# Performance work log

Hardware: AMD Instinct MI355X
Metric: run time of the kernel (lower is better)

Reference implementation:

```python
import jax, jax.numpy as jnp
import numpy as np


def _add_self_loops(src, dst, n):
    loop = jnp.arange(n, dtype=src.dtype)
    return jnp.concatenate([src, loop]), jnp.concatenate([dst, loop])


def _graph_conv(x, src, dst, n, W, b):
    # DGL GraphConv with norm='both':
    #   h = D_in^{-1/2} * A^T * (D_out^{-1/2} * x) @ W + b
    ones = jnp.ones(src.shape, dtype=x.dtype)
    deg_out = jax.ops.segment_sum(ones, src, num_segments=n)
    deg_in = jax.ops.segment_sum(ones, dst, num_segments=n)
    norm_s = jax.lax.rsqrt(jnp.maximum(deg_out, 1.0))
    norm_d = jax.lax.rsqrt(jnp.maximum(deg_in, 1.0))
    msg = (x * norm_s[:, None])[src]                      # [E, d] gather
    agg = jax.ops.segment_sum(msg, dst, num_segments=n)   # [N, d] scatter-add
    return (agg * norm_d[:, None]) @ W + b


def _ntype_forward(x, src, dst, W0, b0, W1, b1):
    n = x.shape[0]
    src, dst = _add_self_loops(src, dst, n)  # dgl.add_self_loop each layer; graph is static
    h = _graph_conv(x, src, dst, n, W0, b0)
    h = jax.nn.relu(h)  # dropout skipped: eval mode (training=False)
    h = _graph_conv(h, src, dst, n, W1, b1)
    return h


def setup_inputs() -> dict:
    key = jax.random.key(0)
    ks = jax.random.split(key, 16)
    NA, NB, EA, EB = 50000, 30000, 600000, 300000
    DA, DB, H = 256, 128, 128
    s = 0.05
    return {
        "feat_a": jax.random.normal(ks[0], (NA, DA), jnp.float32),
        "feat_b": jax.random.normal(ks[1], (NB, DB), jnp.float32),
        "src_a": jax.random.randint(ks[2], (EA,), 0, NA),
        "dst_a": jax.random.randint(ks[3], (EA,), 0, NA),
        "src_b": jax.random.randint(ks[4], (EB,), 0, NB),
        "dst_b": jax.random.randint(ks[5], (EB,), 0, NB),
        "Wa0": jax.random.normal(ks[6], (DA, H), jnp.float32) * s,
        "ba0": jnp.zeros((H,), jnp.float32),
        "Wa1": jax.random.normal(ks[7], (H, H), jnp.float32) * s,
        "ba1": jnp.zeros((H,), jnp.float32),
        "Wb0": jax.random.normal(ks[8], (DB, H), jnp.float32) * s,
        "bb0": jnp.zeros((H,), jnp.float32),
        "Wb1": jax.random.normal(ks[9], (H, H), jnp.float32) * s,
        "bb1": jnp.zeros((H,), jnp.float32),
    }


def reference(feat_a, feat_b, src_a, dst_a, src_b, dst_b,
              Wa0, ba0, Wa1, ba1, Wb0, bb0, Wb1, bb1):
    h_a = _ntype_forward(feat_a, src_a, dst_a, Wa0, ba0, Wa1, ba1)
    h_b = _ntype_forward(feat_b, src_b, dst_b, Wb0, bb0, Wb1, bb1)
    return h_a, h_b
```

## Files before the change

### kernel.cpp

```cpp
#include <hip/hip_runtime.h>
#include <hip/hip_bf16.h>

#define H 128
#define BK 64
#define LDSTR 72

#define EPB 2048
#define BUCK_BITS 8
#define BUCK 256

typedef _Float16 f16;
typedef unsigned int u32;
typedef __attribute__((ext_vector_type(8))) _Float16 f16x8;
typedef __attribute__((ext_vector_type(4))) _Float16 f16x4;
typedef __attribute__((ext_vector_type(4))) float floatx4;

static inline __host__ int ceil_div(int a, int b) { return (a + b - 1) / b; }

__global__ __launch_bounds__(256) void p1K(
    const int* __restrict__ sA, const int* __restrict__ dA, int EA, int nblkA, int nbinsA,
    const int* __restrict__ sB, const int* __restrict__ dB, int EB, int nblkB, int nbinsB,
    int* __restrict__ ch, int offAd, int offBd, int offAs, int offBs, int Lall,
    const float* __restrict__ Wa0, f16* ta0, const float* __restrict__ Wa1, f16* ta1,
    const float* __restrict__ Wb0, f16* tb0, const float* __restrict__ Wb1, f16* tb1, int DA) {
    __shared__ int bd[BUCK], bs[BUCK];
    int bid = blockIdx.x, t = threadIdx.x;
    int p1n = nblkA + nblkB;
    if (bid < p1n) {
        const int *src, *dst; int E, nblk, nbins, blk, od, os;
        if (bid < nblkA) { src = sA; dst = dA; E = EA; nblk = nblkA; nbins = nbinsA; blk = bid; od = offAd; os = offAs; }
        else { src = sB; dst = dB; E = EB; nblk = nblkB; nbins = nbinsB; blk = bid - nblkA; od = offBd; os = offBs; }
        bd[t] = 0; bs[t] = 0;
        __syncthreads();
        int e0 = blk * EPB, e1 = min(E, e0 + EPB);
        for (int e = e0 + t; e < e1; e += 256) {
            atomicAdd(&bd[dst[e] >> BUCK_BITS], 1);
            atomicAdd(&bs[src[e] >> BUCK_BITS], 1);
        }
        __syncthreads();
        for (int b = t; b < nbins; b += 256) {
            ch[od + b * nblk + blk] = bd[b];
            ch[os + b * nblk + blk] = bs[b];
        }
        if (bid == 0 && t == 0) ch[Lall] = 0;
    } else {
        int b2 = bid - p1n;
        int k2 = b2 * 2 + (t >> 7);
        const float* W; f16* T; int D, k;
        if (k2 < DA) { W = Wa0; T = ta0; D = DA; k = k2; }
        else if (k2 < DA + H) { W = Wa1; T = ta1; D = H; k = k2 - DA; }
        else if (k2 < DA + 2 * H) { W = Wb0; T = tb0; D = H; k = k2 - DA - H; }
        else { W = Wb1; T = tb1; D = H; k = k2 - DA - 2 * H; }
        int c = t & 127;
        T[(size_t)c * D + k] = (f16)W[(size_t)k * H + c];
    }
}

__global__ __launch_bounds__(256) void scan1K(int* __restrict__ ch, int n, int* __restrict__ bsum) {
    __shared__ int sh[256];
    int t = threadIdx.x;
    int base = blockIdx.x * 1024 + t * 4;
    int v[4];
#pragma unroll
    for (int i = 0; i < 4; i++) v[i] = (base + i < n) ? ch[base + i] : 0;
    int s = v[0] + v[1] + v[2] + v[3];
    sh[t] = s;
    __syncthreads();
    for (int off = 1; off < 256; off <<= 1) {
        int x = (t >= off) ? sh[t - off] : 0;
        __syncthreads();
        sh[t] += x;
        __syncthreads();
    }
    int run = sh[t] - s;
#pragma unroll
    for (int i = 0; i < 4; i++) {
        if (base + i < n) ch[base + i] = run;
        run += v[i];
    }
    if (t == 255) bsum[blockIdx.x] = sh[255];
}

__global__ __launch_bounds__(256) void scan23K(int* __restrict__ ch, const int* __restrict__ bsum,
                                               int nb, int n) {
    __shared__ int sh[256];
    int t = threadIdx.x;
    int v = (t < nb) ? bsum[t] : 0;
    sh[t] = v;
    __syncthreads();
    for (int off = 1; off < 256; off <<= 1) {
        int x = (t >= off) ? sh[t - off] : 0;
        __syncthreads();
        sh[t] += x;
        __syncthreads();
    }
    int k = blockIdx.x >> 2;
    int add = (k == 0) ? 0 : sh[k - 1];
    int i = blockIdx.x * 256 + t;
    if (i < n) ch[i] += add;
}

__global__ __launch_bounds__(256) void p3K(
    const int* __restrict__ sA, const int* __restrict__ dA, int EA, int nblkA, int nbinsA,
    const int* __restrict__ sB, const int* __restrict__ dB, int EB, int nblkB, int nbinsB,
    const int* __restrict__ ch, int offAd, int offBd, int offAs, int offBs,
    u32* __restrict__ binned) {
    __shared__ int cd[BUCK], cs[BUCK], ofd[BUCK], ofs[BUCK];
    const int *src, *dst; int E, nblk, nbins, blk, od, os;
    if ((int)blockIdx.x < nblkA) {
        src = sA; dst = dA; E = EA; nblk = nblkA; nbins = nbinsA; blk = blockIdx.x; od = offAd; os = offAs;
    } else {
        src = sB; dst = dB; E = EB; nblk = nblkB; nbins = nbinsB; blk = blockIdx.x - nblkA; od = offBd; os = offBs;
    }
    int t = threadIdx.x;
    cd[t] = 0; cs[t] = 0;
    if (t < nbins) {
        ofd[t] = ch[od + t * nblk + blk];
        ofs[t] = ch[os + t * nblk + blk];
    }
    __syncthreads();
    int e0 = blk * EPB, e1 = min(E, e0 + EPB);
    for (int e = e0 + t; e < e1; e += 256) {
        int d = dst[e], s = src[e];
        int b = d >> BUCK_BITS;
        int r = atomicAdd(&cd[b], 1);
        binned[ofd[b] + r] = (u32)s | ((u32)(d & (BUCK - 1)) << 16);
        int b2 = s >> BUCK_BITS;
        int r2 = atomicAdd(&cs[b2], 1);
        binned[ofs[b2] + r2] = (u32)(s & (BUCK - 1));
    }
}

__global__ __launch_bounds__(256) void p4K(
    const u32* __restrict__ binned, const int* __restrict__ ch,
    int nbinsA, int nblkA, int offAd, int offAs,
    int nbinsB, int nblkB, int offBd, int offBs,
    int* __restrict__ rpA, float* __restrict__ ndA, int* __restrict__ esA, int NA, int EA,
    int* __restrict__ rpB, float* __restrict__ ndB, int* __restrict__ esB, int NB, int EB,
    float* __restrict__ nsA, float* __restrict__ nsB) {
    __shared__ int cnt[BUCK], pos[BUCK], fill[BUCK];
    int bid = blockIdx.x, t = threadIdx.x;
    int ndst = nbinsA + nbinsB;
    if (bid == 0 && t == 0) { rpA[NA] = EA; rpB[NB] = EB; }
    if (bid < ndst) {
        int blk, offm, nblkm, N, ebase; int* rp; float* nd; int* es;
        if (bid < nbinsA) { blk = bid; offm = offAd; nblkm = nblkA; rp = rpA; nd = ndA; es = esA; N = NA; ebase = 0; }
        else { blk = bid - nbinsA; offm = offBd; nblkm = nblkB; rp = rpB; nd = ndB; es = esB; N = NB; ebase = EA; }
        int e0 = ch[offm + blk * nblkm];
        int e1 = ch[offm + (blk + 1) * nblkm];
        cnt[t] = 0; fill[t] = 0;
        __syncthreads();
        for (int e = e0 + t; e < e1; e += 256) atomicAdd(&cnt[(binned[e] >> 16) & 255], 1);
        __syncthreads();
        int c = cnt[t];
        int node = (blk << BUCK_BITS) + t;
        if (node < N) nd[node] = rsqrtf((float)(c + 1));
        pos[t] = c;
        __syncthreads();
        for (int off = 1; off < 256; off <<= 1) {
            int x = (t >= off) ? pos[t - off] : 0;
            __syncthreads();
            pos[t] += x;
            __syncthreads();
        }
        int start = e0 + pos[t] - c - ebase;
        pos[t] = start;
        if (node < N) rp[node] = start;
        __syncthreads();
        for (int e = e0 + t; e < e1; e += 256) {
            u32 w = binned[e];
            int i = (w >> 16) & 255;
            int r = atomicAdd(&fill[i], 1);
            es[pos[i] + r] = (int)(w & 0xFFFFu);
        }
    } else {
        int b2 = bid - ndst;
        int blk, offm, nblkm, N; float* ns;
        if (b2 < nbinsA) { blk = b2; offm = offAs; nblkm = nblkA; ns = nsA; N = NA; }
        else { blk = b2 - nbinsA; offm = offBs; nblkm = nblkB; ns = nsB; N = NB; }
        int e0 = ch[offm + blk * nblkm];
        int e1 = ch[offm + (blk + 1) * nblkm];
        cnt[t] = 0;
        __syncthreads();
        for (int e = e0 + t; e < e1; e += 256) atomicAdd(&cnt[binned[e] & 255], 1);
        __syncthreads();
        int node = (blk << BUCK_BITS) + t;
        if (node < N) ns[node] = rsqrtf((float)(cnt[t] + 1));
    }
}

__global__ __launch_bounds__(256) void gemmF(
    const float* __restrict__ X32A, const f16* __restrict__ X16A, const f16* __restrict__ WtA,
    const float* __restrict__ nsA, f16* __restrict__ YA, int NA, int DA, int nblkA,
    const float* __restrict__ X32B, const f16* __restrict__ X16B, const f16* __restrict__ WtB,
    const float* __restrict__ nsB, f16* __restrict__ YB, int NB, int DB, int xf16) {
    const float* X32; const f16* X16; const f16* Wt; const float* ns; f16* Y; int N, D, bid;
    if ((int)blockIdx.x < nblkA) {
        X32 = X32A; X16 = X16A; Wt = WtA; ns = nsA; Y = YA; N = NA; D = DA; bid = blockIdx.x;
    } else {
        X32 = X32B; X16 = X16B; Wt = WtB; ns = nsB; Y = YB; N = NB; D = DB; bid = blockIdx.x - nblkA;
    }
    __shared__ f16 Xs[64 * LDSTR];
    __shared__ f16 Ws[128 * LDSTR];
    int t = threadIdx.x;
    int wv = t >> 6, lane = t & 63;
    int m = lane & 15, q = lane >> 4;
    int rowbase = bid * 64;

    floatx4 acc[8];
#pragma unroll
    for (int c = 0; c < 8; c++) acc[c] = (floatx4)(0.f);

    for (int k0 = 0; k0 < D; k0 += BK) {
        __syncthreads();
        if (xf16) {
            int kq = (t & 7) * 8;
            int r0 = t >> 3;
#pragma unroll
            for (int i = 0; i < 2; i++) {
                int r = r0 + i * 32;
                int grow = rowbase + r;
                f16x8 v = (f16x8)(f16)0;
                if (grow < N) v = *(const f16x8*)(X16 + (size_t)grow * D + k0 + kq);
                *(f16x8*)&Xs[r * LDSTR + kq] = v;
            }
        } else {
            int kq = (t & 15) * 4;
#pragma unroll
            for (int i = 0; i < 4; i++) {
                int r = (t >> 4) + i * 16;
                int grow = rowbase + r;
                float4 v = make_float4(0.f, 0.f, 0.f, 0.f);
                float nv = 0.f;
                if (grow < N) {
                    v = *(const float4*)(X32 + (size_t)grow * D + k0 + kq);
                    nv = ns[grow];
                }
                f16x4 hv;
                hv[0] = (f16)(v.x * nv); hv[1] = (f16)(v.y * nv);
                hv[2] = (f16)(v.z * nv); hv[3] = (f16)(v.w * nv);
                *(f16x4*)&Xs[r * LDSTR + kq] = hv;
            }
        }
        {
            int ks = (t & 7) * 8;
            int rb = t >> 3;
#pragma unroll
            for (int i = 0; i < 4; i++) {
                int c = rb + i * 32;
                *(f16x8*)&Ws[c * LDSTR + ks] = *(const f16x8*)&Wt[(size_t)c * D + k0 + ks];
            }
        }
        __syncthreads();
#pragma unroll
        for (int ks = 0; ks < BK; ks += 32) {
            f16x8 a = *(const f16x8*)&Xs[(wv * 16 + m) * LDSTR + ks + q * 8];
#pragma unroll
            for (int c = 0; c < 8; c++) {
                f16x8 b = *(const f16x8*)&Ws[(c * 16 + m) * LDSTR + ks + q * 8];
                acc[c] = __builtin_amdgcn_mfma_f32_16x16x32_f16(a, b, acc[c], 0, 0, 0);
            }
        }
    }
#pragma unroll
    for (int c = 0; c < 8; c++)
#pragma unroll
        for (int r = 0; r < 4; r++) {
            int grow = rowbase + wv * 16 + q * 4 + r;
            if (grow < N) Y[(size_t)grow * H + c * 16 + m] = (f16)acc[c][r];
        }
}

__global__ __launch_bounds__(256) void aggC(
    const f16* __restrict__ YA, const int* __restrict__ rpA, const int* __restrict__ esA,
    const float* __restrict__ ndA, const float* __restrict__ nsA, const float* __restrict__ bA,
    float* __restrict__ oA, f16* __restrict__ hA, int nA32, int NA,
    const f16* __restrict__ YB, const int* __restrict__ rpB, const int* __restrict__ esB,
    const float* __restrict__ ndB, const float* __restrict__ nsB, const float* __restrict__ bB,
    float* __restrict__ oB, f16* __restrict__ hB, int NB, int layer0) {
    const f16* Y; const int *rp, *es; const float *nd, *ns, *bias; float* out; f16* hout;
    int N, blk;
    if ((int)blockIdx.x < nA32) {
        Y = YA; rp = rpA; es = esA; nd = ndA; ns = nsA; bias = bA; out = oA; hout = hA;
        N = NA; blk = blockIdx.x;
    } else {
        Y = YB; rp = rpB; es = esB; nd = ndB; ns = nsB; bias = bB; out = oB; hout = hB;
        N = NB; blk = blockIdx.x - nA32;
    }
    int t = threadIdx.x;
    int slot = t >> 3;
    int d = t & 7;
    int node = blk * 32 + slot;
    bool act = node < N;
    int nc = act ? node : (N - 1);
    int beg = rp[nc];
    int cnt = act ? (rp[nc + 1] - beg) : 0;
    int tot = cnt + 1;
    const f16* Yd = Y + (size_t)d * 16;
    float acc[16];
#pragma unroll
    for (int i = 0; i < 16; i++) acc[i] = 0.f;
    int i0 = (0 < cnt) ? es[beg]     : nc;
    int i1 = (1 < cnt) ? es[beg + 1] : nc;
    int i2 = (2 < cnt) ? es[beg + 2] : nc;
    int i3 = (3 < cnt) ? es[beg + 3] : nc;
    int j = 0;
    for (; j + 4 <= tot; j += 4) {
        f16x8 a0 = *(const f16x8*)(Yd + (size_t)i0 * H);
        f16x8 b0 = *(const f16x8*)(Yd + (size_t)i0 * H + 8);
        f16x8 a1 = *(const f16x8*)(Yd + (size_t)i1 * H);
        f16x8 b1 = *(const f16x8*)(Yd + (size_t)i1 * H + 8);
        f16x8 a2 = *(const f16x8*)(Yd + (size_t)i2 * H);
        f16x8 b2 = *(const f16x8*)(Yd + (size_t)i2 * H + 8);
        f16x8 a3 = *(const f16x8*)(Yd + (size_t)i3 * H);
        f16x8 b3 = *(const f16x8*)(Yd + (size_t)i3 * H + 8);
        int jn = j + 4;
        int n0 = (jn     < cnt) ? es[beg + jn]     : nc;
        int n1 = (jn + 1 < cnt) ? es[beg + jn + 1] : nc;
        int n2 = (jn + 2 < cnt) ? es[beg + jn + 2] : nc;
        int n3 = (jn + 3 < cnt) ? es[beg + jn + 3] : nc;
#pragma unroll
        for (int i = 0; i < 8; i++) {
            acc[i]     += ((float)a0[i] + (float)a1[i]) + ((float)a2[i] + (float)a3[i]);
            acc[i + 8] += ((float)b0[i] + (float)b1[i]) + ((float)b2[i] + (float)b3[i]);
        }
        i0 = n0; i1 = n1; i2 = n2; i3 = n3;
    }
    int rem = tot - j;
    if (rem > 0) {
        f16x8 a0 = *(const f16x8*)(Yd + (size_t)i0 * H);
        f16x8 b0 = *(const f16x8*)(Yd + (size_t)i0 * H + 8);
        if (rem > 1) {
            f16x8 a1 = *(const f16x8*)(Yd + (size_t)i1 * H);
            f16x8 b1 = *(const f16x8*)(Yd + (size_t)i1 * H + 8);
            if (rem > 2) {
                f16x8 a2 = *(const f16x8*)(Yd + (size_t)i2 * H);
                f16x8 b2 = *(const f16x8*)(Yd + (size_t)i2 * H + 8);
#pragma unroll
                for (int i = 0; i < 8; i++) {
                    acc[i]     += ((float)a0[i] + (float)a1[i]) + (float)a2[i];
                    acc[i + 8] += ((float)b0[i] + (float)b1[i]) + (float)b2[i];
                }
            } else {
#pragma unroll
                for (int i = 0; i < 8; i++) {
                    acc[i]     += (float)a0[i] + (float)a1[i];
                    acc[i + 8] += (float)b0[i] + (float)b1[i];
                }
            }
        } else {
#pragma unroll
            for (int i = 0; i < 8; i++) {
                acc[i]     += (float)a0[i];
                acc[i + 8] += (float)b0[i];
            }
        }
    }
    if (act) {
        float ndv = nd[node];
        float4 c0 = *(const float4*)(bias + d * 16);
        float4 c1 = *(const float4*)(bias + d * 16 + 4);
        float4 c2 = *(const float4*)(bias + d * 16 + 8);
        float4 c3 = *(const float4*)(bias + d * 16 + 12);
        float o_[16];
        o_[0]  = fmaf(acc[0],  ndv, c0.x); o_[1]  = fmaf(acc[1],  ndv, c0.y);
        o_[2]  = fmaf(acc[2],  ndv, c0.z); o_[3]  = fmaf(acc[3],  ndv, c0.w);
        o_[4]  = fmaf(acc[4],  ndv, c1.x); o_[5]  = fmaf(acc[5],  ndv, c1.y);
        o_[6]  = fmaf(acc[6],  ndv, c1.z); o_[7]  = fmaf(acc[7],  ndv, c1.w);
        o_[8]  = fmaf(acc[8],  ndv, c2.x); o_[9]  = fmaf(acc[9],  ndv, c2.y);
        o_[10] = fmaf(acc[10], ndv, c2.z); o_[11] = fmaf(acc[11], ndv, c2.w);
        o_[12] = fmaf(acc[12], ndv, c3.x); o_[13] = fmaf(acc[13], ndv, c3.y);
        o_[14] = fmaf(acc[14], ndv, c3.z); o_[15] = fmaf(acc[15], ndv, c3.w);
        if (layer0) {
            float nsv = ns[node];
            f16x8 h0, h1;
#pragma unroll
            for (int i = 0; i < 8; i++) {
                h0[i] = (f16)(fmaxf(o_[i], 0.f) * nsv);
                h1[i] = (f16)(fmaxf(o_[i + 8], 0.f) * nsv);
            }
            *(f16x8*)(hout + (size_t)node * H + d * 16) = h0;
            *(f16x8*)(hout + (size_t)node * H + d * 16 + 8) = h1;
        } else {
            float* op = out + (size_t)node * H + d * 16;
            *(float4*)op       = make_float4(o_[0],  o_[1],  o_[2],  o_[3]);
            *(float4*)(op + 4) = make_float4(o_[4],  o_[5],  o_[6],  o_[7]);
            *(float4*)(op + 8) = make_float4(o_[8],  o_[9],  o_[10], o_[11]);
            *(float4*)(op + 12)= make_float4(o_[12], o_[13], o_[14], o_[15]);
        }
    }
}


struct TypeBufs {
    int *rowptr, *esrc;
    float *norm_s, *norm_d;
    f16 *h, *y, *wt0, *wt1;
};

extern "C" void kernel_launch(void* const* d_in, const int* in_sizes, int n_in,
                              void* d_out, int out_size, void* d_ws, size_t ws_size,
                              hipStream_t stream) {
    (void)n_in; (void)out_size; (void)ws_size;
    const float* feat_a = (const float*)d_in[0];
    const float* feat_b = (const float*)d_in[1];
    const int* src_a = (const int*)d_in[2];
    const int* dst_a = (const int*)d_in[3];
    const int* src_b = (const int*)d_in[4];
    const int* dst_b = (const int*)d_in[5];
    const float* Wa0 = (const float*)d_in[6];
    const float* ba0 = (const float*)d_in[7];
    const float* Wa1 = (const float*)d_in[8];
    const float* ba1 = (const float*)d_in[9];
    const float* Wb0 = (const float*)d_in[10];
    const float* bb0 = (const float*)d_in[11];
    const float* Wb1 = (const float*)d_in[12];
    const float* bb1 = (const float*)d_in[13];

    const int DA = in_sizes[6] / H;
    const int DB = in_sizes[10] / H;
    const int NA = in_sizes[0] / DA;
    const int NB = in_sizes[1] / DB;
    const int EA = in_sizes[2];
    const int EB = in_sizes[4];

    const int nblkA = ceil_div(EA, EPB), nblkB = ceil_div(EB, EPB);
    const int nbinsA = ceil_div(NA, BUCK), nbinsB = ceil_div(NB, BUCK);
    const int LAd = nbinsA * nblkA, LBd = nbinsB * nblkB;
    const int offAd = 0;
    const int offBd = LAd;
    const int offAs = offBd + LBd;
    const int offBs = offAs + LAd;
    const int Lall = offBs + LBd;

    char* w = (char*)d_ws;
    auto carve = [&](size_t bytes) {
        void* p = (void*)w;
        w += (bytes + 255) & ~(size_t)255;
        return p;
    };
    int* ch = (int*)carve(((size_t)Lall + 1) * 4);
    int* bsum = (int*)carve(256 * 4);
    u32* binned = (u32*)carve((size_t)2 * (EA + EB) * 4);
    auto carve_type = [&](int N, int E, int D) {
        TypeBufs tb;
        tb.rowptr = (int*)carve(((size_t)N + 1) * 4);
        tb.esrc   = (int*)carve((size_t)E * 4);
        tb.norm_s = (float*)carve((size_t)N * 4);
        tb.norm_d = (float*)carve((size_t)N * 4);
        tb.h      = (f16*)carve((size_t)N * H * 2);
        tb.y      = (f16*)carve((size_t)N * H * 2);
        tb.wt0    = (f16*)carve((size_t)D * H * 2);
        tb.wt1    = (f16*)carve((size_t)H * H * 2);
        return tb;
    };
    TypeBufs A = carve_type(NA, EA, DA);
    TypeBufs B = carve_type(NB, EB, DB);

    float* out_a = (float*)d_out;
    float* out_b = out_a + (size_t)NA * H;

    const int gblkA = ceil_div(NA, 64), gblkB = ceil_div(NB, 64);
    const int nA32 = ceil_div(NA, 32), nB32 = ceil_div(NB, 32);
    const int wcBlocks = (DA + 3 * H) / 2;
    const int nScan = Lall + 1;
    const int sb1 = ceil_div(nScan, 1024);

    p1K<<<nblkA + nblkB + wcBlocks, 256, 0, stream>>>(
        src_a, dst_a, EA, nblkA, nbinsA, src_b, dst_b, EB, nblkB, nbinsB,
        ch, offAd, offBd, offAs, offBs, Lall,
        Wa0, A.wt0, Wa1, A.wt1, Wb0, B.wt0, Wb1, B.wt1, DA);
    scan1K<<<sb1, 256, 0, stream>>>(ch, nScan, bsum);
    scan23K<<<ceil_div(nScan, 256), 256, 0, stream>>>(ch, bsum, sb1, nScan);
    p3K<<<nblkA + nblkB, 256, 0, stream>>>(
        src_a, dst_a, EA, nblkA, nbinsA, src_b, dst_b, EB, nblkB, nbinsB,
        ch, offAd, offBd, offAs, offBs, binned);
    p4K<<<2 * (nbinsA + nbinsB), 256, 0, stream>>>(
        binned, ch, nbinsA, nblkA, offAd, offAs, nbinsB, nblkB, offBd, offBs,
        A.rowptr, A.norm_d, A.esrc, NA, EA,
        B.rowptr, B.norm_d, B.esrc, NB, EB,
        A.norm_s, B.norm_s);
    gemmF<<<gblkA + gblkB, 256, 0, stream>>>(
        feat_a, (const f16*)nullptr, A.wt0, A.norm_s, A.y, NA, DA, gblkA,
        feat_b, (const f16*)nullptr, B.wt0, B.norm_s, B.y, NB, DB, 0);
    aggC<<<nA32 + nB32, 256, 0, stream>>>(
        A.y, A.rowptr, A.esrc, A.norm_d, A.norm_s, ba0, out_a, A.h, nA32, NA,
        B.y, B.rowptr, B.esrc, B.norm_d, B.norm_s, bb0, out_b, B.h, NB, 1);
    gemmF<<<gblkA + gblkB, 256, 0, stream>>>(
        (const float*)nullptr, A.h, A.wt1, A.norm_s, A.y, NA, H, gblkA,
        (const float*)nullptr, B.h, B.wt1, B.norm_s, B.y, NB, H, 1);
    aggC<<<nA32 + nB32, 256, 0, stream>>>(
        A.y, A.rowptr, A.esrc, A.norm_d, A.norm_s, ba1, out_a, A.h, nA32, NA,
        B.y, B.rowptr, B.esrc, B.norm_d, B.norm_s, bb1, out_b, B.h, NB, 0);
}
```

Measured before the change: 264.8 us.

## Replace multi-pass counting sort with fixed-capacity global-atomic bucketing

```diff
diff --git a/kernel.cpp b/kernel.cpp
--- a/kernel.cpp
+++ b/kernel.cpp
@@ -5,9 +5,9 @@
 #define BK 64
 #define LDSTR 72
 
-#define EPB 2048
 #define BUCK_BITS 8
 #define BUCK 256
+#define CAP_BITS 13
 
 typedef _Float16 f16;
 typedef unsigned int u32;
@@ -17,34 +17,16 @@
 
 static inline __host__ int ceil_div(int a, int b) { return (a + b - 1) / b; }
 
-__global__ __launch_bounds__(256) void p1K(
-    const int* __restrict__ sA, const int* __restrict__ dA, int EA, int nblkA, int nbinsA,
-    const int* __restrict__ sB, const int* __restrict__ dB, int EB, int nblkB, int nbinsB,
-    int* __restrict__ ch, int offAd, int offBd, int offAs, int offBs, int Lall,
+__global__ __launch_bounds__(256) void zK(
+    int* __restrict__ cnts, int nCnt, int zBlocks,
     const float* __restrict__ Wa0, f16* ta0, const float* __restrict__ Wa1, f16* ta1,
     const float* __restrict__ Wb0, f16* tb0, const float* __restrict__ Wb1, f16* tb1, int DA) {
-    __shared__ int bd[BUCK], bs[BUCK];
     int bid = blockIdx.x, t = threadIdx.x;
-    int p1n = nblkA + nblkB;
-    if (bid < p1n) {
-        const int *src, *dst; int E, nblk, nbins, blk, od, os;
-        if (bid < nblkA) { src = sA; dst = dA; E = EA; nblk = nblkA; nbins = nbinsA; blk = bid; od = offAd; os = offAs; }
-        else { src = sB; dst = dB; E = EB; nblk = nblkB; nbins = nbinsB; blk = bid - nblkA; od = offBd; os = offBs; }
-        bd[t] = 0; bs[t] = 0;
-        __syncthreads();
-        int e0 = blk * EPB, e1 = min(E, e0 + EPB);
-        for (int e = e0 + t; e < e1; e += 256) {
-            atomicAdd(&bd[dst[e] >> BUCK_BITS], 1);
-            atomicAdd(&bs[src[e] >> BUCK_BITS], 1);
-        }
-        __syncthreads();
-        for (int b = t; b < nbins; b += 256) {
-            ch[od + b * nblk + blk] = bd[b];
-            ch[os + b * nblk + blk] = bs[b];
-        }
-        if (bid == 0 && t == 0) ch[Lall] = 0;
+    if (bid < zBlocks) {
+        int i = bid * 256 + t;
+        if (i < nCnt) cnts[i] = 0;
     } else {
-        int b2 = bid - p1n;
+        int b2 = bid - zBlocks;
         int k2 = b2 * 2 + (t >> 7);
         const float* W; f16* T; int D, k;
         if (k2 < DA) { W = Wa0; T = ta0; D = DA; k = k2; }
@@ -56,149 +38,83 @@
     }
 }
 
-__global__ __launch_bounds__(256) void scan1K(int* __restrict__ ch, int n, int* __restrict__ bsum) {
-    __shared__ int sh[256];
-    int t = threadIdx.x;
-    int base = blockIdx.x * 1024 + t * 4;
-    int v[4];
-#pragma unroll
-    for (int i = 0; i < 4; i++) v[i] = (base + i < n) ? ch[base + i] : 0;
-    int s = v[0] + v[1] + v[2] + v[3];
-    sh[t] = s;
+__global__ __launch_bounds__(256) void sK(
+    const int* __restrict__ sA, const int* __restrict__ dA, int EA,
+    const int* __restrict__ sB, const int* __restrict__ dB, int EB,
+    int nbinsA, int* __restrict__ bcnt,
+    int* __restrict__ scntA, int* __restrict__ scntB,
+    u32* __restrict__ binned) {
+    int tot = EA + EB;
+    for (int e = blockIdx.x * 256 + threadIdx.x; e < tot; e += gridDim.x * 256) {
+        int s, d, boff; int* scnt;
+        if (e < EA) { s = sA[e]; d = dA[e]; boff = 0; scnt = scntA; }
+        else { s = sB[e - EA]; d = dB[e - EA]; boff = nbinsA; scnt = scntB; }
+        int b = boff + (d >> BUCK_BITS);
+        int r = atomicAdd(&bcnt[b], 1);
+        binned[((size_t)b << CAP_BITS) + r] = (u32)s | ((u32)(d & (BUCK - 1)) << 16);
+        atomicAdd(&scnt[s], 1);
+    }
+}
+
+__global__ __launch_bounds__(256) void p4K(
+    const u32* __restrict__ binned, const int* __restrict__ bcnt,
+    int nbinsA, int nbinsB,
+    int* __restrict__ rpA, float* __restrict__ ndA, int* __restrict__ esA, int NA, int EA,
+    int* __restrict__ rpB, float* __restrict__ ndB, int* __restrict__ esB, int NB, int EB) {
+    __shared__ int cnt[BUCK], pos[BUCK], fill[BUCK], bases[BUCK];
+    int bid = blockIdx.x, t = threadIdx.x;
+    if (bid == 0 && t == 0) { rpA[NA] = EA; rpB[NB] = EB; }
+    int blk, nbins, boff, N; int* rp; float* nd; int* es;
+    if (bid < nbinsA) { blk = bid; nbins = nbinsA; boff = 0; rp = rpA; nd = ndA; es = esA; N = NA; }
+    else { blk = bid - nbinsA; nbins = nbinsB; boff = nbinsA; rp = rpB; nd = ndB; es = esB; N = NB; }
+    bases[t] = (t < nbins) ? bcnt[boff + t] : 0;
     __syncthreads();
     for (int off = 1; off < 256; off <<= 1) {
-        int x = (t >= off) ? sh[t - off] : 0;
-        __syncthreads();
-        sh[t] += x;
-        __syncthreads();
-    }
-    int run = sh[t] - s;
-#pragma unroll
-    for (int i = 0; i < 4; i++) {
-        if (base + i < n) ch[base + i] = run;
-        run += v[i];
-    }
-    if (t == 255) bsum[blockIdx.x] = sh[255];
-}
-
-__global__ __launch_bounds__(256) void scan23K(int* __restrict__ ch, const int* __restrict__ bsum,
-                                               int nb, int n) {
-    __shared__ int sh[256];
-    int t = threadIdx.x;
-    int v = (t < nb) ? bsum[t] : 0;
-    sh[t] = v;
+        int x = (t >= off) ? bases[t - off] : 0;
+        __syncthreads();
+        bases[t] += x;
+        __syncthreads();
+    }
+    int base = (blk == 0) ? 0 : bases[blk - 1];
+    int count = bases[blk] - base;
+    const u32* bp = binned + ((size_t)(boff + blk) << CAP_BITS);
+    cnt[t] = 0; fill[t] = 0;
+    __syncthreads();
+    for (int e = t; e < count; e += 256) atomicAdd(&cnt[(bp[e] >> 16) & 255], 1);
+    __syncthreads();
+    int c = cnt[t];
+    int node = (blk << BUCK_BITS) + t;
+    if (node < N) nd[node] = rsqrtf((float)(c + 1));
+    pos[t] = c;
     __syncthreads();
     for (int off = 1; off < 256; off <<= 1) {
-        int x = (t >= off) ? sh[t - off] : 0;
-        __syncthreads();
-        sh[t] += x;
-        __syncthreads();
-    }
-    int k = blockIdx.x >> 2;
-    int add = (k == 0) ? 0 : sh[k - 1];
-    int i = blockIdx.x * 256 + t;
-    if (i < n) ch[i] += add;
-}
-
-__global__ __launch_bounds__(256) void p3K(
-    const int* __restrict__ sA, const int* __restrict__ dA, int EA, int nblkA, int nbinsA,
-    const int* __restrict__ sB, const int* __restrict__ dB, int EB, int nblkB, int nbinsB,
-    const int* __restrict__ ch, int offAd, int offBd, int offAs, int offBs,
-    u32* __restrict__ binned) {
-    __shared__ int cd[BUCK], cs[BUCK], ofd[BUCK], ofs[BUCK];
-    const int *src, *dst; int E, nblk, nbins, blk, od, os;
-    if ((int)blockIdx.x < nblkA) {
-        src = sA; dst = dA; E = EA; nblk = nblkA; nbins = nbinsA; blk = blockIdx.x; od = offAd; os = offAs;
-    } else {
-        src = sB; dst = dB; E = EB; nblk = nblkB; nbins = nbinsB; blk = blockIdx.x - nblkA; od = offBd; os = offBs;
-    }
-    int t = threadIdx.x;
-    cd[t] = 0; cs[t] = 0;
-    if (t < nbins) {
-        ofd[t] = ch[od + t * nblk + blk];
-        ofs[t] = ch[os + t * nblk + blk];
-    }
+        int x = (t >= off) ? pos[t - off] : 0;
+        __syncthreads();
+        pos[t] += x;
+        __syncthreads();
+    }
+    int start = base + pos[t] - c;
+    pos[t] = start;
+    if (node < N) rp[node] = start;
     __syncthreads();
-    int e0 = blk * EPB, e1 = min(E, e0 + EPB);
-    for (int e = e0 + t; e < e1; e += 256) {
-        int d = dst[e], s = src[e];
-        int b = d >> BUCK_BITS;
-        int r = atomicAdd(&cd[b], 1);
-        binned[ofd[b] + r] = (u32)s | ((u32)(d & (BUCK - 1)) << 16);
-        int b2 = s >> BUCK_BITS;
-        int r2 = atomicAdd(&cs[b2], 1);
-        binned[ofs[b2] + r2] = (u32)(s & (BUCK - 1));
-    }
-}
-
-__global__ __launch_bounds__(256) void p4K(
-    const u32* __restrict__ binned, const int* __restrict__ ch,
-    int nbinsA, int nblkA, int offAd, int offAs,
-    int nbinsB, int nblkB, int offBd, int offBs,
-    int* __restrict__ rpA, float* __restrict__ ndA, int* __restrict__ esA, int NA, int EA,
-    int* __restrict__ rpB, float* __restrict__ ndB, int* __restrict__ esB, int NB, int EB,
-    float* __restrict__ nsA, float* __restrict__ nsB) {
-    __shared__ int cnt[BUCK], pos[BUCK], fill[BUCK];
-    int bid = blockIdx.x, t = threadIdx.x;
-    int ndst = nbinsA + nbinsB;
-    if (bid == 0 && t == 0) { rpA[NA] = EA; rpB[NB] = EB; }
-    if (bid < ndst) {
-        int blk, offm, nblkm, N, ebase; int* rp; float* nd; int* es;
-        if (bid < nbinsA) { blk = bid; offm = offAd; nblkm = nblkA; rp = rpA; nd = ndA; es = esA; N = NA; ebase = 0; }
-        else { blk = bid - nbinsA; offm = offBd; nblkm = nblkB; rp = rpB; nd = ndB; es = esB; N = NB; ebase = EA; }
-        int e0 = ch[offm + blk * nblkm];
-        int e1 = ch[offm + (blk + 1) * nblkm];
-        cnt[t] = 0; fill[t] = 0;
-        __syncthreads();
-        for (int e = e0 + t; e < e1; e += 256) atomicAdd(&cnt[(binned[e] >> 16) & 255], 1);
-        __syncthreads();
-        int c = cnt[t];
-        int node = (blk << BUCK_BITS) + t;
-        if (node < N) nd[node] = rsqrtf((float)(c + 1));
-        pos[t] = c;
-        __syncthreads();
-        for (int off = 1; off < 256; off <<= 1) {
-            int x = (t >= off) ? pos[t - off] : 0;
-            __syncthreads();
-            pos[t] += x;
-            __syncthreads();
-        }
-        int start = e0 + pos[t] - c - ebase;
-        pos[t] = start;
-        if (node < N) rp[node] = start;
-        __syncthreads();
-        for (int e = e0 + t; e < e1; e += 256) {
-            u32 w = binned[e];
-            int i = (w >> 16) & 255;
-            int r = atomicAdd(&fill[i], 1);
-            es[pos[i] + r] = (int)(w & 0xFFFFu);
-        }
-    } else {
-        int b2 = bid - ndst;
-        int blk, offm, nblkm, N; float* ns;
-        if (b2 < nbinsA) { blk = b2; offm = offAs; nblkm = nblkA; ns = nsA; N = NA; }
-        else { blk = b2 - nbinsA; offm = offBs; nblkm = nblkB; ns = nsB; N = NB; }
-        int e0 = ch[offm + blk * nblkm];
-        int e1 = ch[offm + (blk + 1) * nblkm];
-        cnt[t] = 0;
-        __syncthreads();
-        for (int e = e0 + t; e < e1; e += 256) atomicAdd(&cnt[binned[e] & 255], 1);
-        __syncthreads();
-        int node = (blk << BUCK_BITS) + t;
-        if (node < N) ns[node] = rsqrtf((float)(cnt[t] + 1));
+    for (int e = t; e < count; e += 256) {
+        u32 w = bp[e];
+        int i = (w >> 16) & 255;
+        int r = atomicAdd(&fill[i], 1);
+        es[pos[i] + r] = (int)(w & 0xFFFFu);
     }
 }
 
 __global__ __launch_bounds__(256) void gemmF(
     const float* __restrict__ X32A, const f16* __restrict__ X16A, const f16* __restrict__ WtA,
-    const float* __restrict__ nsA, f16* __restrict__ YA, int NA, int DA, int nblkA,
+    const int* __restrict__ csA, f16* __restrict__ YA, int NA, int DA, int nblkA,
     const float* __restrict__ X32B, const f16* __restrict__ X16B, const f16* __restrict__ WtB,
-    const float* __restrict__ nsB, f16* __restrict__ YB, int NB, int DB, int xf16) {
-    const float* X32; const f16* X16; const f16* Wt; const float* ns; f16* Y; int N, D, bid;
+    const int* __restrict__ csB, f16* __restrict__ YB, int NB, int DB, int xf16) {
+    const float* X32; const f16* X16; const f16* Wt; const int* cs; f16* Y; int N, D, bid;
     if ((int)blockIdx.x < nblkA) {
-        X32 = X32A; X16 = X16A; Wt = WtA; ns = nsA; Y = YA; N = NA; D = DA; bid = blockIdx.x;
+        X32 = X32A; X16 = X16A; Wt = WtA; cs = csA; Y = YA; N = NA; D = DA; bid = blockIdx.x;
     } else {
-        X32 = X32B; X16 = X16B; Wt = WtB; ns = nsB; Y = YB; N = NB; D = DB; bid = blockIdx.x - nblkA;
+        X32 = X32B; X16 = X16B; Wt = WtB; cs = csB; Y = YB; N = NB; D = DB; bid = blockIdx.x - nblkA;
     }
     __shared__ f16 Xs[64 * LDSTR];
     __shared__ f16 Ws[128 * LDSTR];
@@ -234,7 +150,7 @@
                 float nv = 0.f;
                 if (grow < N) {
                     v = *(const float4*)(X32 + (size_t)grow * D + k0 + kq);
-                    nv = ns[grow];
+                    nv = rsqrtf((float)cs[grow] + 1.0f);
                 }
                 f16x4 hv;
                 hv[0] = (f16)(v.x * nv); hv[1] = (f16)(v.y * nv);
@@ -273,18 +189,18 @@
 
 __global__ __launch_bounds__(256) void aggC(
     const f16* __restrict__ YA, const int* __restrict__ rpA, const int* __restrict__ esA,
-    const float* __restrict__ ndA, const float* __restrict__ nsA, const float* __restrict__ bA,
+    const float* __restrict__ ndA, const int* __restrict__ csA, const float* __restrict__ bA,
     float* __restrict__ oA, f16* __restrict__ hA, int nA32, int NA,
     const f16* __restrict__ YB, const int* __restrict__ rpB, const int* __restrict__ esB,
-    const float* __restrict__ ndB, const float* __restrict__ nsB, const float* __restrict__ bB,
+    const float* __restrict__ ndB, const int* __restrict__ csB, const float* __restrict__ bB,
     float* __restrict__ oB, f16* __restrict__ hB, int NB, int layer0) {
-    const f16* Y; const int *rp, *es; const float *nd, *ns, *bias; float* out; f16* hout;
+    const f16* Y; const int *rp, *es, *cs; const float *nd, *bias; float* out; f16* hout;
     int N, blk;
     if ((int)blockIdx.x < nA32) {
-        Y = YA; rp = rpA; es = esA; nd = ndA; ns = nsA; bias = bA; out = oA; hout = hA;
+        Y = YA; rp = rpA; es = esA; nd = ndA; cs = csA; bias = bA; out = oA; hout = hA;
         N = NA; blk = blockIdx.x;
     } else {
-        Y = YB; rp = rpB; es = esB; nd = ndB; ns = nsB; bias = bB; out = oB; hout = hB;
+        Y = YB; rp = rpB; es = esB; nd = ndB; cs = csB; bias = bB; out = oB; hout = hB;
         N = NB; blk = blockIdx.x - nA32;
     }
     int t = threadIdx.x;
@@ -372,7 +288,7 @@
         o_[12] = fmaf(acc[12], ndv, c3.x); o_[13] = fmaf(acc[13], ndv, c3.y);
         o_[14] = fmaf(acc[14], ndv, c3.z); o_[15] = fmaf(acc[15], ndv, c3.w);
         if (layer0) {
-            float nsv = ns[node];
+            float nsv = rsqrtf((float)cs[node] + 1.0f);
             f16x8 h0, h1;
 #pragma unroll
             for (int i = 0; i < 8; i++) {
@@ -394,7 +310,7 @@
 
 struct TypeBufs {
     int *rowptr, *esrc;
-    float *norm_s, *norm_d;
+    float *norm_d;
     f16 *h, *y, *wt0, *wt1;
 };
 
@@ -424,14 +340,9 @@
     const int EA = in_sizes[2];
     const int EB = in_sizes[4];
 
-    const int nblkA = ceil_div(EA, EPB), nblkB = ceil_div(EB, EPB);
     const int nbinsA = ceil_div(NA, BUCK), nbinsB = ceil_div(NB, BUCK);
-    const int LAd = nbinsA * nblkA, LBd = nbinsB * nblkB;
-    const int offAd = 0;
-    const int offBd = LAd;
-    const int offAs = offBd + LBd;
-    const int offBs = offAs + LAd;
-    const int Lall = offBs + LBd;
+    const int nbins = nbinsA + nbinsB;
+    const int nCnt = nbins + NA + NB;
 
     char* w = (char*)d_ws;
     auto carve = [&](size_t bytes) {
@@ -439,14 +350,15 @@
         w += (bytes + 255) & ~(size_t)255;
         return p;
     };
-    int* ch = (int*)carve(((size_t)Lall + 1) * 4);
-    int* bsum = (int*)carve(256 * 4);
-    u32* binned = (u32*)carve((size_t)2 * (EA + EB) * 4);
+    int* cnts = (int*)carve((size_t)nCnt * 4);
+    int* bcnt = cnts;
+    int* scntA = cnts + nbins;
+    int* scntB = cnts + nbins + NA;
+    u32* binned = (u32*)carve(((size_t)nbins << CAP_BITS) * 4);
     auto carve_type = [&](int N, int E, int D) {
         TypeBufs tb;
         tb.rowptr = (int*)carve(((size_t)N + 1) * 4);
         tb.esrc   = (int*)carve((size_t)E * 4);
-        tb.norm_s = (float*)carve((size_t)N * 4);
         tb.norm_d = (float*)carve((size_t)N * 4);
         tb.h      = (f16*)carve((size_t)N * H * 2);
         tb.y      = (f16*)carve((size_t)N * H * 2);
@@ -463,33 +375,28 @@
     const int gblkA = ceil_div(NA, 64), gblkB = ceil_div(NB, 64);
     const int nA32 = ceil_div(NA, 32), nB32 = ceil_div(NB, 32);
     const int wcBlocks = (DA + 3 * H) / 2;
-    const int nScan = Lall + 1;
-    const int sb1 = ceil_div(nScan, 1024);
-
-    p1K<<<nblkA + nblkB + wcBlocks, 256, 0, stream>>>(
-        src_a, dst_a, EA, nblkA, nbinsA, src_b, dst_b, EB, nblkB, nbinsB,
-        ch, offAd, offBd, offAs, offBs, Lall,
+    const int zBlocks = ceil_div(nCnt, 256);
+
+    zK<<<zBlocks + wcBlocks, 256, 0, stream>>>(
+        cnts, nCnt, zBlocks,
         Wa0, A.wt0, Wa1, A.wt1, Wb0, B.wt0, Wb1, B.wt1, DA);
-    scan1K<<<sb1, 256, 0, stream>>>(ch, nScan, bsum);
-    scan23K<<<ceil_div(nScan, 256), 256, 0, stream>>>(ch, bsum, sb1, nScan);
-    p3K<<<nblkA + nblkB, 256, 0, stream>>>(
-        src_a, dst_a, EA, nblkA, nbinsA, src_b, dst_b, EB, nblkB, nbinsB,
-        ch, offAd, offBd, offAs, offBs, binned);
-    p4K<<<2 * (nbinsA + nbinsB), 256, 0, stream>>>(
-        binned, ch, nbinsA, nblkA, offAd, offAs, nbinsB, nblkB, offBd, offBs,
+    sK<<<2048, 256, 0, stream>>>(
+        src_a, dst_a, EA, src_b, dst_b, EB,
+        nbinsA, bcnt, scntA, scntB, binned);
+    p4K<<<nbins, 256, 0, stream>>>(
+        binned, bcnt, nbinsA, nbinsB,
         A.rowptr, A.norm_d, A.esrc, NA, EA,
-        B.rowptr, B.norm_d, B.esrc, NB, EB,
-        A.norm_s, B.norm_s);
+        B.rowptr, B.norm_d, B.esrc, NB, EB);
     gemmF<<<gblkA + gblkB, 256, 0, stream>>>(
-        feat_a, (const f16*)nullptr, A.wt0, A.norm_s, A.y, NA, DA, gblkA,
-        feat_b, (const f16*)nullptr, B.wt0, B.norm_s, B.y, NB, DB, 0);
+        feat_a, (const f16*)nullptr, A.wt0, scntA, A.y, NA, DA, gblkA,
+        feat_b, (const f16*)nullptr, B.wt0, scntB, B.y, NB, DB, 0);
     aggC<<<nA32 + nB32, 256, 0, stream>>>(
-        A.y, A.rowptr, A.esrc, A.norm_d, A.norm_s, ba0, out_a, A.h, nA32, NA,
-        B.y, B.rowptr, B.esrc, B.norm_d, B.norm_s, bb0, out_b, B.h, NB, 1);
+        A.y, A.rowptr, A.esrc, A.norm_d, scntA, ba0, out_a, A.h, nA32, NA,
+        B.y, B.rowptr, B.esrc, B.norm_d, scntB, bb0, out_b, B.h, NB, 1);
     gemmF<<<gblkA + gblkB, 256, 0, stream>>>(
-        (const float*)nullptr, A.h, A.wt1, A.norm_s, A.y, NA, H, gblkA,
-        (const float*)nullptr, B.h, B.wt1, B.norm_s, B.y, NB, H, 1);
+        (const float*)nullptr, A.h, A.wt1, scntA, A.y, NA, H, gblkA,
+        (const float*)nullptr, B.h, B.wt1, scntB, B.y, NB, H, 1);
     aggC<<<nA32 + nB32, 256, 0, stream>>>(
-        A.y, A.rowptr, A.esrc, A.norm_d, A.norm_s, ba1, out_a, A.h, nA32, NA,
-        B.y, B.rowptr, B.esrc, B.norm_d, B.norm_s, bb1, out_b, B.h, NB, 0);
-}
+        A.y, A.rowptr, A.esrc, A.norm_d, scntA, ba1, out_a, A.h, nA32, NA,
+        B.y, B.rowptr, B.esrc, B.norm_d, scntB, bb1, out_b, B.h, NB, 0);
+}
```

Result: slower. 739.3 us (+179.2%).

## Compute out-degree with global atomics instead of binning source edges

Applied to the files above, without the earlier changes.

```diff
diff --git a/kernel.cpp b/kernel.cpp
--- a/kernel.cpp
+++ b/kernel.cpp
@@ -17,34 +17,16 @@
 
 static inline __host__ int ceil_div(int a, int b) { return (a + b - 1) / b; }
 
-__global__ __launch_bounds__(256) void p1K(
-    const int* __restrict__ sA, const int* __restrict__ dA, int EA, int nblkA, int nbinsA,
-    const int* __restrict__ sB, const int* __restrict__ dB, int EB, int nblkB, int nbinsB,
-    int* __restrict__ ch, int offAd, int offBd, int offAs, int offBs, int Lall,
+__global__ __launch_bounds__(256) void zK(
+    int* __restrict__ cnts, int nCnt, int zBlocks,
     const float* __restrict__ Wa0, f16* ta0, const float* __restrict__ Wa1, f16* ta1,
     const float* __restrict__ Wb0, f16* tb0, const float* __restrict__ Wb1, f16* tb1, int DA) {
-    __shared__ int bd[BUCK], bs[BUCK];
     int bid = blockIdx.x, t = threadIdx.x;
-    int p1n = nblkA + nblkB;
-    if (bid < p1n) {
-        const int *src, *dst; int E, nblk, nbins, blk, od, os;
-        if (bid < nblkA) { src = sA; dst = dA; E = EA; nblk = nblkA; nbins = nbinsA; blk = bid; od = offAd; os = offAs; }
-        else { src = sB; dst = dB; E = EB; nblk = nblkB; nbins = nbinsB; blk = bid - nblkA; od = offBd; os = offBs; }
-        bd[t] = 0; bs[t] = 0;
-        __syncthreads();
-        int e0 = blk * EPB, e1 = min(E, e0 + EPB);
-        for (int e = e0 + t; e < e1; e += 256) {
-            atomicAdd(&bd[dst[e] >> BUCK_BITS], 1);
-            atomicAdd(&bs[src[e] >> BUCK_BITS], 1);
-        }
-        __syncthreads();
-        for (int b = t; b < nbins; b += 256) {
-            ch[od + b * nblk + blk] = bd[b];
-            ch[os + b * nblk + blk] = bs[b];
-        }
-        if (bid == 0 && t == 0) ch[Lall] = 0;
+    if (bid < zBlocks) {
+        int i = bid * 256 + t;
+        if (i < nCnt) cnts[i] = 0;
     } else {
-        int b2 = bid - p1n;
+        int b2 = bid - zBlocks;
         int k2 = b2 * 2 + (t >> 7);
         const float* W; f16* T; int D, k;
         if (k2 < DA) { W = Wa0; T = ta0; D = DA; k = k2; }
@@ -56,6 +38,28 @@
     }
 }
 
+__global__ __launch_bounds__(256) void p1K(
+    const int* __restrict__ sA, const int* __restrict__ dA, int EA, int nblkA, int nbinsA,
+    const int* __restrict__ sB, const int* __restrict__ dB, int EB, int nblkB, int nbinsB,
+    int* __restrict__ ch, int offAd, int offBd, int Lall,
+    int* __restrict__ scntA, int* __restrict__ scntB) {
+    __shared__ int bd[BUCK];
+    int bid = blockIdx.x, t = threadIdx.x;
+    const int *src, *dst; int E, nblk, nbins, blk, od; int* scnt;
+    if (bid < nblkA) { src = sA; dst = dA; E = EA; nblk = nblkA; nbins = nbinsA; blk = bid; od = offAd; scnt = scntA; }
+    else { src = sB; dst = dB; E = EB; nblk = nblkB; nbins = nbinsB; blk = bid - nblkA; od = offBd; scnt = scntB; }
+    bd[t] = 0;
+    __syncthreads();
+    int e0 = blk * EPB, e1 = min(E, e0 + EPB);
+    for (int e = e0 + t; e < e1; e += 256) {
+        atomicAdd(&bd[dst[e] >> BUCK_BITS], 1);
+        atomicAdd(&scnt[src[e]], 1);
+    }
+    __syncthreads();
+    for (int b = t; b < nbins; b += 256) ch[od + b * nblk + blk] = bd[b];
+    if (bid == 0 && t == 0) ch[Lall] = 0;
+}
+
 __global__ __launch_bounds__(256) void scan1K(int* __restrict__ ch, int n, int* __restrict__ bsum) {
     __shared__ int sh[256];
     int t = threadIdx.x;
@@ -103,21 +107,18 @@
 __global__ __launch_bounds__(256) void p3K(
     const int* __restrict__ sA, const int* __restrict__ dA, int EA, int nblkA, int nbinsA,
     const int* __restrict__ sB, const int* __restrict__ dB, int EB, int nblkB, int nbinsB,
-    const int* __restrict__ ch, int offAd, int offBd, int offAs, int offBs,
+    const int* __restrict__ ch, int offAd, int offBd,
     u32* __restrict__ binned) {
-    __shared__ int cd[BUCK], cs[BUCK], ofd[BUCK], ofs[BUCK];
-    const int *src, *dst; int E, nblk, nbins, blk, od, os;
+    __shared__ int cd[BUCK], ofd[BUCK];
+    const int *src, *dst; int E, nblk, nbins, blk, od;
     if ((int)blockIdx.x < nblkA) {
-        src = sA; dst = dA; E = EA; nblk = nblkA; nbins = nbinsA; blk = blockIdx.x; od = offAd; os = offAs;
+        src = sA; dst = dA; E = EA; nblk = nblkA; nbins = nbinsA; blk = blockIdx.x; od = offAd;
     } else {
-        src = sB; dst = dB; E = EB; nblk = nblkB; nbins = nbinsB; blk = blockIdx.x - nblkA; od = offBd; os = offBs;
+        src = sB; dst = dB; E = EB; nblk = nblkB; nbins = nbinsB; blk = blockIdx.x - nblkA; od = offBd;
     }
     int t = threadIdx.x;
-    cd[t] = 0; cs[t] = 0;
-    if (t < nbins) {
-        ofd[t] = ch[od + t * nblk + blk];
-        ofs[t] = ch[os + t * nblk + blk];
-    }
+    cd[t] = 0;
+    if (t < nbins) ofd[t] = ch[od + t * nblk + blk];
     __syncthreads();
     int e0 = blk * EPB, e1 = min(E, e0 + EPB);
     for (int e = e0 + t; e < e1; e += 256) {
@@ -125,80 +126,60 @@
         int b = d >> BUCK_BITS;
         int r = atomicAdd(&cd[b], 1);
         binned[ofd[b] + r] = (u32)s | ((u32)(d & (BUCK - 1)) << 16);
-        int b2 = s >> BUCK_BITS;
-        int r2 = atomicAdd(&cs[b2], 1);
-        binned[ofs[b2] + r2] = (u32)(s & (BUCK - 1));
     }
 }
 
 __global__ __launch_bounds__(256) void p4K(
     const u32* __restrict__ binned, const int* __restrict__ ch,
-    int nbinsA, int nblkA, int offAd, int offAs,
-    int nbinsB, int nblkB, int offBd, int offBs,
+    int nbinsA, int nblkA, int offAd,
+    int nbinsB, int nblkB, int offBd,
     int* __restrict__ rpA, float* __restrict__ ndA, int* __restrict__ esA, int NA, int EA,
-    int* __restrict__ rpB, float* __restrict__ ndB, int* __restrict__ esB, int NB, int EB,
-    float* __restrict__ nsA, float* __restrict__ nsB) {
+    int* __restrict__ rpB, float* __restrict__ ndB, int* __restrict__ esB, int NB, int EB) {
     __shared__ int cnt[BUCK], pos[BUCK], fill[BUCK];
     int bid = blockIdx.x, t = threadIdx.x;
-    int ndst = nbinsA + nbinsB;
     if (bid == 0 && t == 0) { rpA[NA] = EA; rpB[NB] = EB; }
-    if (bid < ndst) {
-        int blk, offm, nblkm, N, ebase; int* rp; float* nd; int* es;
-        if (bid < nbinsA) { blk = bid; offm = offAd; nblkm = nblkA; rp = rpA; nd = ndA; es = esA; N = NA; ebase = 0; }
-        else { blk = bid - nbinsA; offm = offBd; nblkm = nblkB; rp = rpB; nd = ndB; es = esB; N = NB; ebase = EA; }
-        int e0 = ch[offm + blk * nblkm];
-        int e1 = ch[offm + (blk + 1) * nblkm];
-        cnt[t] = 0; fill[t] = 0;
-        __syncthreads();
-        for (int e = e0 + t; e < e1; e += 256) atomicAdd(&cnt[(binned[e] >> 16) & 255], 1);
-        __syncthreads();
-        int c = cnt[t];
-        int node = (blk << BUCK_BITS) + t;
-        if (node < N) nd[node] = rsqrtf((float)(c + 1));
-        pos[t] = c;
-        __syncthreads();
-        for (int off = 1; off < 256; off <<= 1) {
-            int x = (t >= off) ? pos[t - off] : 0;
-            __syncthreads();
-            pos[t] += x;
-            __syncthreads();
-        }
-        int start = e0 + pos[t] - c - ebase;
-        pos[t] = start;
-        if (node < N) rp[node] = start;
-        __syncthreads();
-        for (int e = e0 + t; e < e1; e += 256) {
-            u32 w = binned[e];
-            int i = (w >> 16) & 255;
-            int r = atomicAdd(&fill[i], 1);
-            es[pos[i] + r] = (int)(w & 0xFFFFu);
-        }
-    } else {
-        int b2 = bid - ndst;
-        int blk, offm, nblkm, N; float* ns;
-        if (b2 < nbinsA) { blk = b2; offm = offAs; nblkm = nblkA; ns = nsA; N = NA; }
-        else { blk = b2 - nbinsA; offm = offBs; nblkm = nblkB; ns = nsB; N = NB; }
-        int e0 = ch[offm + blk * nblkm];
-        int e1 = ch[offm + (blk + 1) * nblkm];
-        cnt[t] = 0;
-        __syncthreads();
-        for (int e = e0 + t; e < e1; e += 256) atomicAdd(&cnt[binned[e] & 255], 1);
-        __syncthreads();
-        int node = (blk << BUCK_BITS) + t;
-        if (node < N) ns[node] = rsqrtf((float)(cnt[t] + 1));
+    int blk, offm, nblkm, N, ebase; int* rp; float* nd; int* es;
+    if (bid < nbinsA) { blk = bid; offm = offAd; nblkm = nblkA; rp = rpA; nd = ndA; es = esA; N = NA; ebase = 0; }
+    else { blk = bid - nbinsA; offm = offBd; nblkm = nblkB; rp = rpB; nd = ndB; es = esB; N = NB; ebase = EA; }
+    int e0 = ch[offm + blk * nblkm];
+    int e1 = ch[offm + (blk + 1) * nblkm];
+    cnt[t] = 0; fill[t] = 0;
+    __syncthreads();
+    for (int e = e0 + t; e < e1; e += 256) atomicAdd(&cnt[(binned[e] >> 16) & 255], 1);
+    __syncthreads();
+    int c = cnt[t];
+    int node = (blk << BUCK_BITS) + t;
+    if (node < N) nd[node] = rsqrtf((float)(c + 1));
+    pos[t] = c;
+    __syncthreads();
+    for (int off = 1; off < 256; off <<= 1) {
+        int x = (t >= off) ? pos[t - off] : 0;
+        __syncthreads();
+        pos[t] += x;
+        __syncthreads();
+    }
+    int start = e0 + pos[t] - c - ebase;
+    pos[t] = start;
+    if (node < N) rp[node] = start;
+    __syncthreads();
+    for (int e = e0 + t; e < e1; e += 256) {
+        u32 w = binned[e];
+        int i = (w >> 16) & 255;
+        int r = atomicAdd(&fill[i], 1);
+        es[pos[i] + r] = (int)(w & 0xFFFFu);
     }
 }
 
 __global__ __launch_bounds__(256) void gemmF(
     const float* __restrict__ X32A, const f16* __restrict__ X16A, const f16* __restrict__ WtA,
-    const float* __restrict__ nsA, f16* __restrict__ YA, int NA, int DA, int nblkA,
+    const int* __restrict__ csA, f16* __restrict__ YA, int NA, int DA, int nblkA,
     const float* __restrict__ X32B, const f16* __restrict__ X16B, const f16* __restrict__ WtB,
-    const float* __restrict__ nsB, f16* __restrict__ YB, int NB, int DB, int xf16) {
-    const float* X32; const f16* X16; const f16* Wt; const float* ns; f16* Y; int N, D, bid;
+    const int* __restrict__ csB, f16* __restrict__ YB, int NB, int DB, int xf16) {
+    const float* X32; const f16* X16; const f16* Wt; const int* cs; f16* Y; int N, D, bid;
     if ((int)blockIdx.x < nblkA) {
-        X32 = X32A; X16 = X16A; Wt = WtA; ns = nsA; Y = YA; N = NA; D = DA; bid = blockIdx.x;
+        X32 = X32A; X16 = X16A; Wt = WtA; cs = csA; Y = YA; N = NA; D = DA; bid = blockIdx.x;
     } else {
-        X32 = X32B; X16 = X16B; Wt = WtB; ns = nsB; Y = YB; N = NB; D = DB; bid = blockIdx.x - nblkA;
+        X32 = X32B; X16 = X16B; Wt = WtB; cs = csB; Y = YB; N = NB; D = DB; bid = blockIdx.x - nblkA;
     }
     __shared__ f16 Xs[64 * LDSTR];
     __shared__ f16 Ws[128 * LDSTR];
@@ -234,7 +215,7 @@
                 float nv = 0.f;
                 if (grow < N) {
                     v = *(const float4*)(X32 + (size_t)grow * D + k0 + kq);
-                    nv = ns[grow];
+                    nv = rsqrtf((float)cs[grow] + 1.0f);
                 }
                 f16x4 hv;
                 hv[0] = (f16)(v.x * nv); hv[1] = (f16)(v.y * nv);
@@ -273,18 +254,18 @@
 
 __global__ __launch_bounds__(256) void aggC(
     const f16* __restrict__ YA, const int* __restrict__ rpA, const int* __restrict__ esA,
-    const float* __restrict__ ndA, const float* __restrict__ nsA, const float* __restrict__ bA,
+    const float* __restrict__ ndA, const int* __restrict__ csA, const float* __restrict__ bA,
     float* __restrict__ oA, f16* __restrict__ hA, int nA32, int NA,
     const f16* __restrict__ YB, const int* __restrict__ rpB, const int* __restrict__ esB,
-    const float* __restrict__ ndB, const float* __restrict__ nsB, const float* __restrict__ bB,
+    const float* __restrict__ ndB, const int* __restrict__ csB, const float* __restrict__ bB,
     float* __restrict__ oB, f16* __restrict__ hB, int NB, int layer0) {
-    const f16* Y; const int *rp, *es; const float *nd, *ns, *bias; float* out; f16* hout;
+    const f16* Y; const int *rp, *es, *cs; const float *nd, *bias; float* out; f16* hout;
     int N, blk;
     if ((int)blockIdx.x < nA32) {
-        Y = YA; rp = rpA; es = esA; nd = ndA; ns = nsA; bias = bA; out = oA; hout = hA;
+        Y = YA; rp = rpA; es = esA; nd = ndA; cs = csA; bias = bA; out = oA; hout = hA;
         N = NA; blk = blockIdx.x;
     } else {
-        Y = YB; rp = rpB; es = esB; nd = ndB; ns = nsB; bias = bB; out = oB; hout = hB;
+        Y = YB; rp = rpB; es = esB; nd = ndB; cs = csB; bias = bB; out = oB; hout = hB;
         N = NB; blk = blockIdx.x - nA32;
     }
     int t = threadIdx.x;
@@ -372,7 +353,7 @@
         o_[12] = fmaf(acc[12], ndv, c3.x); o_[13] = fmaf(acc[13], ndv, c3.y);
         o_[14] = fmaf(acc[14], ndv, c3.z); o_[15] = fmaf(acc[15], ndv, c3.w);
         if (layer0) {
-            float nsv = ns[node];
+            float nsv = rsqrtf((float)cs[node] + 1.0f);
             f16x8 h0, h1;
 #pragma unroll
             for (int i = 0; i < 8; i++) {
@@ -394,7 +375,7 @@
 
 struct TypeBufs {
     int *rowptr, *esrc;
-    float *norm_s, *norm_d;
+    float *norm_d;
     f16 *h, *y, *wt0, *wt1;
 };
 
@@ -429,9 +410,7 @@
     const int LAd = nbinsA * nblkA, LBd = nbinsB * nblkB;
     const int offAd = 0;
     const int offBd = LAd;
-    const int offAs = offBd + LBd;
-    const int offBs = offAs + LAd;
-    const int Lall = offBs + LBd;
+    const int Lall = offBd + LBd;
 
     char* w = (char*)d_ws;
     auto carve = [&](size_t bytes) {
@@ -441,12 +420,13 @@
     };
     int* ch = (int*)carve(((size_t)Lall + 1) * 4);
     int* bsum = (int*)carve(256 * 4);
-    u32* binned = (u32*)carve((size_t)2 * (EA + EB) * 4);
+    int* scntA = (int*)carve((size_t)(NA + NB) * 4);
+    int* scntB = scntA + NA;
+    u32* binned = (u32*)carve((size_t)(EA + EB) * 4);
     auto carve_type = [&](int N, int E, int D) {
         TypeBufs tb;
         tb.rowptr = (int*)carve(((size_t)N + 1) * 4);
         tb.esrc   = (int*)carve((size_t)E * 4);
-        tb.norm_s = (float*)carve((size_t)N * 4);
         tb.norm_d = (float*)carve((size_t)N * 4);
         tb.h      = (f16*)carve((size_t)N * H * 2);
         tb.y      = (f16*)carve((size_t)N * H * 2);
@@ -463,33 +443,35 @@
     const int gblkA = ceil_div(NA, 64), gblkB = ceil_div(NB, 64);
     const int nA32 = ceil_div(NA, 32), nB32 = ceil_div(NB, 32);
     const int wcBlocks = (DA + 3 * H) / 2;
+    const int zBlocks = ceil_div(NA + NB, 256);
     const int nScan = Lall + 1;
     const int sb1 = ceil_div(nScan, 1024);
 
-    p1K<<<nblkA + nblkB + wcBlocks, 256, 0, stream>>>(
+    zK<<<zBlocks + wcBlocks, 256, 0, stream>>>(
+        scntA, NA + NB, zBlocks,
+        Wa0, A.wt0, Wa1, A.wt1, Wb0, B.wt0, Wb1, B.wt1, DA);
+    p1K<<<nblkA + nblkB, 256, 0, stream>>>(
         src_a, dst_a, EA, nblkA, nbinsA, src_b, dst_b, EB, nblkB, nbinsB,
-        ch, offAd, offBd, offAs, offBs, Lall,
-        Wa0, A.wt0, Wa1, A.wt1, Wb0, B.wt0, Wb1, B.wt1, DA);
+        ch, offAd, offBd, Lall, scntA, scntB);
     scan1K<<<sb1, 256, 0, stream>>>(ch, nScan, bsum);
     scan23K<<<ceil_div(nScan, 256), 256, 0, stream>>>(ch, bsum, sb1, nScan);
     p3K<<<nblkA + nblkB, 256, 0, stream>>>(
         src_a, dst_a, EA, nblkA, nbinsA, src_b, dst_b, EB, nblkB, nbinsB,
-        ch, offAd, offBd, offAs, offBs, binned);
-    p4K<<<2 * (nbinsA + nbinsB), 256, 0, stream>>>(
-        binned, ch, nbinsA, nblkA, offAd, offAs, nbinsB, nblkB, offBd, offBs,
+        ch, offAd, offBd, binned);
+    p4K<<<nbinsA + nbinsB, 256, 0, stream>>>(
+        binned, ch, nbinsA, nblkA, offAd, nbinsB, nblkB, offBd,
         A.rowptr, A.norm_d, A.esrc, NA, EA,
-        B.rowptr, B.norm_d, B.esrc, NB, EB,
-        A.norm_s, B.norm_s);
+        B.rowptr, B.norm_d, B.esrc, NB, EB);
     gemmF<<<gblkA + gblkB, 256, 0, stream>>>(
-        feat_a, (const f16*)nullptr, A.wt0, A.norm_s, A.y, NA, DA, gblkA,
-        feat_b, (const f16*)nullptr, B.wt0, B.norm_s, B.y, NB, DB, 0);
+        feat_a, (const f16*)nullptr, A.wt0, scntA, A.y, NA, DA, gblkA,
+        feat_b, (const f16*)nullptr, B.wt0, scntB, B.y, NB, DB, 0);
     aggC<<<nA32 + nB32, 256, 0, stream>>>(
-        A.y, A.rowptr, A.esrc, A.norm_d, A.norm_s, ba0, out_a, A.h, nA32, NA,
-        B.y, B.rowptr, B.esrc, B.norm_d, B.norm_s, bb0, out_b, B.h, NB, 1);
+        A.y, A.rowptr, A.esrc, A.norm_d, scntA, ba0, out_a, A.h, nA32, NA,
+        B.y, B.rowptr, B.esrc, B.norm_d, scntB, bb0, out_b, B.h, NB, 1);
     gemmF<<<gblkA + gblkB, 256, 0, stream>>>(
-        (const float*)nullptr, A.h, A.wt1, A.norm_s, A.y, NA, H, gblkA,
-        (const float*)nullptr, B.h, B.wt1, B.norm_s, B.y, NB, H, 1);
+        (const float*)nullptr, A.h, A.wt1, scntA, A.y, NA, H, gblkA,
+        (const float*)nullptr, B.h, B.wt1, scntB, B.y, NB, H, 1);
     aggC<<<nA32 + nB32, 256, 0, stream>>>(
-        A.y, A.rowptr, A.esrc, A.norm_d, A.norm_s, ba1, out_a, A.h, nA32, NA,
-        B.y, B.rowptr, B.esrc, B.norm_d, B.norm_s, bb1, out_b, B.h, NB, 0);
-}
+        A.y, A.rowptr, A.esrc, A.norm_d, scntA, ba1, out_a, A.h, nA32, NA,
+        B.y, B.rowptr, B.esrc, B.norm_d, scntB, bb1, out_b, B.h, NB, 0);
+}
```

After: 288.5 us. 9.0% more time.
